# Performance work log

Measured on AMD Instinct MI355X. Metric: run time of the kernel, lower is better.

## Reference

```python
import jax, jax.numpy as jnp
import numpy as np

DT = 0.001          # time step (s)
DX = 5.0            # grid spacing x (m)
DY = 5.0            # grid spacing y (m)
FD_PAD = 2          # accuracy=4 -> stencil half-width 2
PML_W = 20          # default pml_width
PAD = FD_PAD + PML_W
PML_FREQ = 25.0     # default dominant frequency for PML
NZ, NY = 250, 350
N_SHOTS, N_SRC, NT = 4, 1, 48
N_RECV = 100


def _shift(w, k, axis):
    """result[i] = w[i+k] along axis, zero fill outside."""
    pad = [(0, 0)] * w.ndim
    sl = [slice(None)] * w.ndim
    if k >= 0:
        pad[axis] = (0, k)
        sl[axis] = slice(k, None)
    else:
        pad[axis] = (-k, 0)
        sl[axis] = slice(None, k)
    return jnp.pad(w[tuple(sl)], pad)


def _d1(w, axis, d):
    # 4th-order central first derivative
    return (8.0 * (_shift(w, 1, axis) - _shift(w, -1, axis))
            - (_shift(w, 2, axis) - _shift(w, -2, axis))) / (12.0 * d)


def _d2(w, axis, d):
    # 4th-order central second derivative
    return (-(_shift(w, 2, axis) + _shift(w, -2, axis))
            + 16.0 * (_shift(w, 1, axis) + _shift(w, -1, axis))
            - 30.0 * w) / (12.0 * d * d)


def _pml_profiles(n, width, d, dt, vmax, freq):
    """C-PML decay (b) and update (a) coefficients along one axis."""
    x = jnp.arange(n, dtype=jnp.float32)
    frac_lo = jnp.clip((FD_PAD + width - x) / width, 0.0, 1.0)
    frac_hi = jnp.clip((x - (n - 1 - FD_PAD - width)) / width, 0.0, 1.0)
    frac = jnp.maximum(frac_lo, frac_hi)          # 0 interior -> 1 at edge
    sigma = 3.0 * vmax * jnp.log(1000.0) / (2.0 * width * d) * frac * frac
    alpha = jnp.pi * freq * (1.0 - frac)
    b = jnp.exp(-(sigma + alpha) * dt)
    a = sigma / (sigma + alpha + 1e-9) * (b - 1.0)
    return a.astype(jnp.float32), b.astype(jnp.float32)


def setup_inputs() -> dict:
    key = jax.random.key(0)
    k1, k2, k3, k4, k5, k6, k7 = jax.random.split(key, 7)
    v = 1500.0 + 1000.0 * jax.random.uniform(k1, (NZ, NY), jnp.float32)
    scatter = 0.1 * jax.random.normal(k2, (NZ, NY), jnp.float32)
    source_amplitudes = jax.random.normal(k3, (N_SHOTS, N_SRC, NT), jnp.float32)
    source_locations = jnp.stack([
        jax.random.randint(k4, (N_SHOTS, N_SRC), 0, NZ),
        jax.random.randint(k5, (N_SHOTS, N_SRC), 0, NY)], axis=-1)
    receiver_locations = jnp.stack([
        jax.random.randint(k6, (N_SHOTS, N_RECV), 0, NZ),
        jax.random.randint(k7, (N_SHOTS, N_RECV), 0, NY)], axis=-1)
    return {"v": v, "scatter": scatter, "source_amplitudes": source_amplitudes,
            "source_locations": source_locations,
            "receiver_locations": receiver_locations}


def reference(v, scatter, source_amplitudes, source_locations, receiver_locations):
    vp = jnp.pad(v, PAD, mode='edge')              # replicate-pad velocity
    sp = jnp.pad(scatter, PAD)                     # zero-pad scatter
    nx, ny = vp.shape
    vmax = jax.lax.stop_gradient(jnp.max(jnp.abs(v)))
    ax, bx = _pml_profiles(nx, PML_W, DX, DT, vmax, PML_FREQ)
    ay, by = _pml_profiles(ny, PML_W, DY, DT, vmax, PML_FREQ)
    ax, bx = ax[:, None], bx[:, None]              # broadcast over y
    ay, by = ay[None, :], by[None, :]              # broadcast over x
    v2dt2 = vp * vp * (DT * DT)

    n, n_src, nt = source_amplitudes.shape
    sl = source_locations + PAD
    rl = receiver_locations + PAD
    shot = jnp.arange(n)[:, None]
    sx, sy = sl[..., 0], sl[..., 1]
    rx, ry = rl[..., 0], rl[..., 1]

    z = jnp.zeros((n, nx, ny), v.dtype)
    carry0 = (z,) * 12
    amps = jnp.moveaxis(source_amplitudes, -1, 0)  # [nt, shot, src]

    def pml_laplacian(wfc, px, py, zx, zy):
        px = bx * px + ax * _d1(wfc, 1, DX)
        py = by * py + ay * _d1(wfc, 2, DY)
        tx = _d2(wfc, 1, DX) + _d1(px, 1, DX)
        ty = _d2(wfc, 2, DY) + _d1(py, 2, DY)
        zx = bx * zx + ax * tx
        zy = by * zy + ay * ty
        return tx + zx + ty + zy, px, py, zx, zy

    def step(carry, amp):
        wfc, wfp, px, py, zx, zy, wsc, wpsc, pxs, pys, zxs, zys = carry
        lap, px, py, zx, zy = pml_laplacian(wfc, px, py, zx, zy)
        wfn = v2dt2 * lap + 2.0 * wfc - wfp
        wfn = wfn.at[shot, sx, sy].add(v2dt2[sx, sy] * amp)
        lapsc, pxs, pys, zxs, zys = pml_laplacian(wsc, pxs, pys, zxs, zys)
        wfnsc = (v2dt2 * lapsc + 2.0 * wsc - wpsc
                 + 2.0 * vp * sp * (DT * DT) * lap)   # Born scattering source
        rec = wfnsc[shot, rx, ry]                      # [shot, receiver]
        return (wfn, wfc, px, py, zx, zy,
                wfnsc, wsc, pxs, pys, zxs, zys), rec

    _, recs = jax.lax.scan(step, carry0, amps)
    receiver_amplitudes = jnp.moveaxis(recs, 0, -1)    # [shot, receiver, time]
    return receiver_amplitudes
```

## Files before the change

kernel.cpp:

```cpp
#include <hip/hip_runtime.h>

#define DTF   0.001f
#define NZV   250
#define NYV   350
#define NX    294
#define NYW   394
#define PADC  22
#define NSHOT 4
#define NTS   48
#define NRECV 100
#define NCELL (NX*NYW)
#define NTOT  (NSHOT*NCELL)
#define XBL   22
#define XBH   (NX-22)
#define YBH   (NYW-22)
#define NB    44
#define PXSZ  (NSHOT*NB*NYW)
#define PYSZ  (NSHOT*NX*NB)
#define NSB   ((NTOT+255)/256)
#define GB    2

__device__ __forceinline__ int xbi(int i) {
    return ((unsigned)i < XBL) ? i : ((i >= XBH && i < NX) ? i-(NX-NB) : -1);
}
__device__ __forceinline__ int ybi(int j) {
    return ((unsigned)j < XBL) ? j : ((j >= YBH && j < NYW) ? j-(NYW-NB) : -1);
}

__device__ __forceinline__ float ldz(const float* __restrict__ w, int i, int j) {
    return ((unsigned)i < (unsigned)NX && (unsigned)j < (unsigned)NYW) ? w[i*NYW + j] : 0.f;
}
__device__ __forceinline__ float d1x(const float* __restrict__ w, int i, int j) {
    return (8.f*(ldz(w,i+1,j) - ldz(w,i-1,j)) - (ldz(w,i+2,j) - ldz(w,i-2,j))) * (1.f/60.f);
}
__device__ __forceinline__ float d1y(const float* __restrict__ w, int i, int j) {
    return (8.f*(ldz(w,i,j+1) - ldz(w,i,j-1)) - (ldz(w,i,j+2) - ldz(w,i,j-2))) * (1.f/60.f);
}
__device__ __forceinline__ float d2x(const float* __restrict__ w, int i, int j, float cc) {
    return (-(ldz(w,i+2,j)+ldz(w,i-2,j)) + 16.f*(ldz(w,i+1,j)+ldz(w,i-1,j)) - 30.f*cc) * (1.f/300.f);
}
__device__ __forceinline__ float d2y(const float* __restrict__ w, int i, int j, float cc) {
    return (-(ldz(w,i,j+2)+ldz(w,i,j-2)) + 16.f*(ldz(w,i,j+1)+ldz(w,i,j-1)) - 30.f*cc) * (1.f/300.f);
}

__global__ void k_vmax(const float* __restrict__ v, unsigned* __restrict__ vmx) {
    __shared__ float sm[256];
    float m = 0.f;
    for (int idx = blockIdx.x*256 + threadIdx.x; idx < NZV*NYV; idx += gridDim.x*256)
        m = fmaxf(m, fabsf(v[idx]));
    sm[threadIdx.x] = m; __syncthreads();
    for (int o = 128; o > 0; o >>= 1) {
        if (threadIdx.x < o) sm[threadIdx.x] = fmaxf(sm[threadIdx.x], sm[threadIdx.x+o]);
        __syncthreads();
    }
    if (threadIdx.x == 0) atomicMax(vmx, __float_as_uint(sm[0]));
}

__global__ void k_prep(const float* __restrict__ v, const float* __restrict__ sc,
                       float* __restrict__ v2dt2, float* __restrict__ sterm) {
    int c = blockIdx.x*blockDim.x + threadIdx.x;
    if (c >= NCELL) return;
    int i = c / NYW, j = c - (c / NYW)*NYW;
    int iz = min(max(i - PADC, 0), NZV-1);
    int iy = min(max(j - PADC, 0), NYV-1);
    float vv = v[iz*NYV + iy];
    v2dt2[c] = vv*vv*(DTF*DTF);
    float sp = 0.f;
    if (i >= PADC && i < PADC+NZV && j >= PADC && j < PADC+NYV)
        sp = sc[(i-PADC)*NYV + (j-PADC)];
    sterm[c] = 2.f*vv*sp*(DTF*DTF);
}

__device__ __forceinline__ void prof1(int x, int n, float d, float vmax, float* a, float* b) {
    float fl = fminf(fmaxf((float)(2 + 20 - x)/20.f, 0.f), 1.f);
    float fh = fminf(fmaxf((float)(x - (n - 23))/20.f, 0.f), 1.f);
    float fr = fmaxf(fl, fh);
    float sigma = 3.f*vmax*logf(1000.f)/(2.f*20.f*d)*fr*fr;
    float alpha = 3.14159265358979f*25.f*(1.f - fr);
    float bb = expf(-(sigma+alpha)*DTF);
    *a = sigma/(sigma+alpha+1e-9f)*(bb-1.f);
    *b = bb;
}

__global__ void k_prof(const unsigned* __restrict__ vmx,
                       float* __restrict__ axv, float* __restrict__ bxv,
                       float* __restrict__ ayv, float* __restrict__ byv) {
    int x = threadIdx.x;
    float vmax = __uint_as_float(vmx[0]);
    if (x < NX)  prof1(x, NX,  5.0f, vmax, &axv[x], &bxv[x]);
    if (x < NYW) prof1(x, NYW, 5.0f, vmax, &ayv[x], &byv[x]);
}

__global__ __launch_bounds__(256) void k_fstep(
    const float* __restrict__ wf,   float* __restrict__ wold,
    const float* __restrict__ wsf,  float* __restrict__ wsold,
    const float* __restrict__ pxo,  float* __restrict__ pxn,
    const float* __restrict__ pyo,  float* __restrict__ pyn,
    const float* __restrict__ pxso, float* __restrict__ pxsn,
    const float* __restrict__ pyso, float* __restrict__ pysn,
    float* __restrict__ zx,  float* __restrict__ zy,
    float* __restrict__ zxs, float* __restrict__ zys,
    const float* __restrict__ v2, const float* __restrict__ st,
    const float* __restrict__ axv, const float* __restrict__ bxv,
    const float* __restrict__ ayv, const float* __restrict__ byv,
    const float* __restrict__ amp, const int* __restrict__ sloc,
    const int* __restrict__ rloc, float* __restrict__ out, int t)
{
    int bid = blockIdx.x;
    if (bid >= NSB) {
        if (t == 0) return;
        int g = (bid - NSB)*256 + threadIdx.x;
        if (g >= NSHOT*NRECV) return;
        int s = g / NRECV, rr = g - s*NRECV;
        int ri = rloc[(s*NRECV+rr)*2+0] + PADC;
        int rj = rloc[(s*NRECV+rr)*2+1] + PADC;
        out[(s*NRECV+rr)*NTS + (t-1)] = wsf[s*NCELL + ri*NYW + rj];
        return;
    }
    int c = bid*256 + threadIdx.x;
    if (c >= NTOT) return;
    int s = c / NCELL; int r = c - s*NCELL;
    int i = r / NYW;   int j = r - i*NYW;

    const float* w  = wf  + s*NCELL;
    const float* ww = wsf + s*NCELL;

    float wc  = w[r];
    float wsc = ww[r];

    float tx  = d2x(w,  i, j, wc);
    float txs = d2x(ww, i, j, wsc);
    float ty  = d2y(w,  i, j, wc);
    float tys = d2y(ww, i, j, wsc);

    int ib = xbi(i);
    int jb = ybi(j);

    if (i <= XBL+1 || i >= XBH-2) {
        float pv[5], pvs[5];
        #pragma unroll
        for (int k = 0; k < 5; ++k) {
            int ik = i + k - 2; int b = xbi(ik);
            float p = 0.f, ps = 0.f;
            if (b >= 0) {
                float bxk = bxv[ik], axk = axv[ik];
                int o = (s*NB + b)*NYW + j;
                p  = bxk*pxo[o]  + axk*d1x(w,  ik, j);
                ps = bxk*pxso[o] + axk*d1x(ww, ik, j);
            }
            pv[k] = p; pvs[k] = ps;
        }
        tx  += (8.f*(pv[3]-pv[1])  - (pv[4]-pv[0]))  * (1.f/60.f);
        txs += (8.f*(pvs[3]-pvs[1]) - (pvs[4]-pvs[0])) * (1.f/60.f);
        if (ib >= 0) {
            int o = (s*NB + ib)*NYW + j;
            pxn[o] = pv[2]; pxsn[o] = pvs[2];
        }
    }

    if (j <= XBL+1 || j >= YBH-2) {
        float pv[5], pvs[5];
        #pragma unroll
        for (int k = 0; k < 5; ++k) {
            int jk = j + k - 2; int b = ybi(jk);
            float p = 0.f, ps = 0.f;
            if (b >= 0) {
                float byk = byv[jk], ayk = ayv[jk];
                int o = (s*NX + i)*NB + b;
                p  = byk*pyo[o]  + ayk*d1y(w,  i, jk);
                ps = byk*pyso[o] + ayk*d1y(ww, i, jk);
            }
            pv[k] = p; pvs[k] = ps;
        }
        ty  += (8.f*(pv[3]-pv[1])  - (pv[4]-pv[0]))  * (1.f/60.f);
        tys += (8.f*(pvs[3]-pvs[1]) - (pvs[4]-pvs[0])) * (1.f/60.f);
        if (jb >= 0) {
            int o = (s*NX + i)*NB + jb;
            pyn[o] = pv[2]; pysn[o] = pvs[2];
        }
    }

    float zxv = 0.f, zyv = 0.f, zxsv = 0.f, zysv = 0.f;
    if (ib >= 0) {
        int o = (s*NB + ib)*NYW + j;
        float bx = bxv[i], ax = axv[i];
        zxv  = bx*zx[o]  + ax*tx;  zx[o]  = zxv;
        zxsv = bx*zxs[o] + ax*txs; zxs[o] = zxsv;
    }
    if (jb >= 0) {
        int o = (s*NX + i)*NB + jb;
        float by = byv[j], ay = ayv[j];
        zyv  = by*zy[o]  + ay*ty;  zy[o]  = zyv;
        zysv = by*zys[o] + ay*tys; zys[o] = zysv;
    }

    float lap  = tx + zxv + ty + zyv;
    float laps = txs + zxsv + tys + zysv;
    float vd   = v2[r];
    float wn   = vd*lap + 2.f*wc - wold[c];
    if (i == sloc[s*2] + PADC && j == sloc[s*2+1] + PADC)
        wn += vd * amp[s*NTS + t];
    float wsn = vd*laps + 2.f*wsc - wsold[c] + st[r]*lap;
    wold[c]  = wn;
    wsold[c] = wsn;
}

__global__ void k_gtail(const float* __restrict__ wsn, const int* __restrict__ rloc,
                        float* __restrict__ out) {
    int g = blockIdx.x*blockDim.x + threadIdx.x;
    if (g >= NSHOT*NRECV) return;
    int s = g / NRECV, rr = g - s*NRECV;
    int ri = rloc[(s*NRECV+rr)*2+0] + PADC;
    int rj = rloc[(s*NRECV+rr)*2+1] + PADC;
    out[(s*NRECV+rr)*NTS + (NTS-1)] = wsn[s*NCELL + ri*NYW + rj];
}

extern "C" void kernel_launch(void* const* d_in, const int* in_sizes, int n_in,
                              void* d_out, int out_size, void* d_ws, size_t ws_size,
                              hipStream_t stream) {
    const float* v    = (const float*)d_in[0];
    const float* scat = (const float*)d_in[1];
    const float* amp  = (const float*)d_in[2];
    const int*   sloc = (const int*)d_in[3];
    const int*   rloc = (const int*)d_in[4];
    float* out = (float*)d_out;
    float* ws  = (float*)d_ws;

    const size_t F = (size_t)NTOT;
    float* wA   = ws;
    float* wB   = wA + F;
    float* sA   = wB + F;
    float* sB   = sA + F;
    float* pxA  = sB + F;
    float* pxB  = pxA + PXSZ;
    float* pxsA = pxB + PXSZ;
    float* pxsB = pxsA + PXSZ;
    float* zx   = pxsB + PXSZ;
    float* zxs  = zx + PXSZ;
    float* pyA  = zxs + PXSZ;
    float* pyB  = pyA + PYSZ;
    float* pysA = pyB + PYSZ;
    float* pysB = pysA + PYSZ;
    float* zy   = pysB + PYSZ;
    float* zys  = zy + PYSZ;
    float* vmxf = zys + PYSZ;
    float* v2   = vmxf + 1;
    float* st   = v2 + NCELL;
    float* axv  = st + NCELL;
    float* bxv  = axv + NX;
    float* ayv  = bxv + NX;
    float* byv  = ayv + NYW;
    unsigned* vmx = (unsigned*)vmxf;

    size_t zero_floats = 4*F + 6*(size_t)PXSZ + 6*(size_t)PYSZ + 1;
    hipMemsetAsync(ws, 0, zero_floats*sizeof(float), stream);

    hipLaunchKernelGGL(k_vmax, dim3(64), dim3(256), 0, stream, v, vmx);
    hipLaunchKernelGGL(k_prep, dim3((NCELL+255)/256), dim3(256), 0, stream, v, scat, v2, st);
    hipLaunchKernelGGL(k_prof, dim3(1), dim3(512), 0, stream, vmx, axv, bxv, ayv, byv);

    float* wc  = wA;  float* wp  = wB;
    float* scc = sA;  float* scp = sB;
    float* pxc = pxA; float* pxn = pxB;
    float* pyc = pyA; float* pyn = pyB;
    float* pxsc = pxsA; float* pxsn = pxsB;
    float* pysc = pysA; float* pysn = pysB;

    for (int t = 0; t < NTS; ++t) {
        hipLaunchKernelGGL(k_fstep, dim3(NSB + GB), dim3(256), 0, stream,
                           wc, wp, scc, scp,
                           pxc, pxn, pyc, pyn, pxsc, pxsn, pysc, pysn,
                           zx, zy, zxs, zys,
                           v2, st, axv, bxv, ayv, byv,
                           amp, sloc, rloc, out, t);
        float* tmp;
        tmp = wc;  wc  = wp;  wp  = tmp;
        tmp = scc; scc = scp; scp = tmp;
        tmp = pxc; pxc = pxn; pxn = tmp;
        tmp = pyc; pyc = pyn; pyn = tmp;
        tmp = pxsc; pxsc = pxsn; pxsn = tmp;
        tmp = pysc; pysc = pysn; pysn = tmp;
    }
    hipLaunchKernelGGL(k_gtail, dim3(2), dim3(256), 0, stream, scc, rloc, out);
}
```

Baseline: 602.8 us.

## Compute four adjacent y-cells per thread to reuse stencil loads in registers

Each thread of the step kernel now handles four consecutive y-cells of one row. It loads a shared row window into registers and reuses it for the y second derivative and the y PML derivatives, instead of issuing separate bounds-checked loads per cell. This cuts the number of threads and the redundant neighbour loads, but raises register pressure, leaves threads uncoalesced across the strided j groups, and adds a wide workspace offset for the vmax slot.

```diff
diff --git a/kernel.cpp b/kernel.cpp
--- a/kernel.cpp
+++ b/kernel.cpp
@@ -17,8 +17,12 @@
 #define NB    44
 #define PXSZ  (NSHOT*NB*NYW)
 #define PYSZ  (NSHOT*NX*NB)
-#define NSB   ((NTOT+255)/256)
+#define NTHR  256
+#define NJG   99
+#define WITEMS (NSHOT*NX*NJG)
+#define NSB2  ((WITEMS+255)/256)
 #define GB    2
+#define BARF  1024
 
 __device__ __forceinline__ int xbi(int i) {
     return ((unsigned)i < XBL) ? i : ((i >= XBH && i < NX) ? i-(NX-NB) : -1);
@@ -26,21 +30,18 @@
 __device__ __forceinline__ int ybi(int j) {
     return ((unsigned)j < XBL) ? j : ((j >= YBH && j < NYW) ? j-(NYW-NB) : -1);
 }
-
 __device__ __forceinline__ float ldz(const float* __restrict__ w, int i, int j) {
     return ((unsigned)i < (unsigned)NX && (unsigned)j < (unsigned)NYW) ? w[i*NYW + j] : 0.f;
 }
-__device__ __forceinline__ float d1x(const float* __restrict__ w, int i, int j) {
-    return (8.f*(ldz(w,i+1,j) - ldz(w,i-1,j)) - (ldz(w,i+2,j) - ldz(w,i-2,j))) * (1.f/60.f);
-}
-__device__ __forceinline__ float d1y(const float* __restrict__ w, int i, int j) {
-    return (8.f*(ldz(w,i,j+1) - ldz(w,i,j-1)) - (ldz(w,i,j+2) - ldz(w,i,j-2))) * (1.f/60.f);
-}
-__device__ __forceinline__ float d2x(const float* __restrict__ w, int i, int j, float cc) {
-    return (-(ldz(w,i+2,j)+ldz(w,i-2,j)) + 16.f*(ldz(w,i+1,j)+ldz(w,i-1,j)) - 30.f*cc) * (1.f/300.f);
-}
-__device__ __forceinline__ float d2y(const float* __restrict__ w, int i, int j, float cc) {
-    return (-(ldz(w,i,j+2)+ldz(w,i,j-2)) + 16.f*(ldz(w,i,j+1)+ldz(w,i,j-1)) - 30.f*cc) * (1.f/300.f);
+__device__ __forceinline__ void prof1(int x, int n, float d, float vmax, float* a, float* b) {
+    float fl = fminf(fmaxf((float)(2 + 20 - x)/20.f, 0.f), 1.f);
+    float fh = fminf(fmaxf((float)(x - (n - 23))/20.f, 0.f), 1.f);
+    float fr = fmaxf(fl, fh);
+    float sigma = 3.f*vmax*logf(1000.f)/(2.f*20.f*d)*fr*fr;
+    float alpha = 3.14159265358979f*25.f*(1.f - fr);
+    float bb = expf(-(sigma+alpha)*DTF);
+    *a = sigma/(sigma+alpha+1e-9f)*(bb-1.f);
+    *b = bb;
 }
 
 __global__ void k_vmax(const float* __restrict__ v, unsigned* __restrict__ vmx) {
@@ -71,17 +72,6 @@
     sterm[c] = 2.f*vv*sp*(DTF*DTF);
 }
 
-__device__ __forceinline__ void prof1(int x, int n, float d, float vmax, float* a, float* b) {
-    float fl = fminf(fmaxf((float)(2 + 20 - x)/20.f, 0.f), 1.f);
-    float fh = fminf(fmaxf((float)(x - (n - 23))/20.f, 0.f), 1.f);
-    float fr = fmaxf(fl, fh);
-    float sigma = 3.f*vmax*logf(1000.f)/(2.f*20.f*d)*fr*fr;
-    float alpha = 3.14159265358979f*25.f*(1.f - fr);
-    float bb = expf(-(sigma+alpha)*DTF);
-    *a = sigma/(sigma+alpha+1e-9f)*(bb-1.f);
-    *b = bb;
-}
-
 __global__ void k_prof(const unsigned* __restrict__ vmx,
                        float* __restrict__ axv, float* __restrict__ bxv,
                        float* __restrict__ ayv, float* __restrict__ byv) {
@@ -91,7 +81,7 @@
     if (x < NYW) prof1(x, NYW, 5.0f, vmax, &ayv[x], &byv[x]);
 }
 
-__global__ __launch_bounds__(256) void k_fstep(
+__global__ __launch_bounds__(256) void k_fstep4(
     const float* __restrict__ wf,   float* __restrict__ wold,
     const float* __restrict__ wsf,  float* __restrict__ wsold,
     const float* __restrict__ pxo,  float* __restrict__ pxn,
@@ -107,9 +97,9 @@
     const int* __restrict__ rloc, float* __restrict__ out, int t)
 {
     int bid = blockIdx.x;
-    if (bid >= NSB) {
+    if (bid >= NSB2) {
         if (t == 0) return;
-        int g = (bid - NSB)*256 + threadIdx.x;
+        int g = (bid - NSB2)*256 + threadIdx.x;
         if (g >= NSHOT*NRECV) return;
         int s = g / NRECV, rr = g - s*NRECV;
         int ri = rloc[(s*NRECV+rr)*2+0] + PADC;
@@ -117,92 +107,141 @@
         out[(s*NRECV+rr)*NTS + (t-1)] = wsf[s*NCELL + ri*NYW + rj];
         return;
     }
-    int c = bid*256 + threadIdx.x;
-    if (c >= NTOT) return;
-    int s = c / NCELL; int r = c - s*NCELL;
-    int i = r / NYW;   int j = r - i*NYW;
+    int g = bid*256 + threadIdx.x;
+    if (g >= WITEMS) return;
+    int s  = g / (NX*NJG);
+    int rm = g - s*(NX*NJG);
+    int i  = rm / NJG;
+    int jg = rm - i*NJG;
+    int j0 = jg*4;
 
     const float* w  = wf  + s*NCELL;
     const float* ww = wsf + s*NCELL;
 
-    float wc  = w[r];
-    float wsc = ww[r];
-
-    float tx  = d2x(w,  i, j, wc);
-    float txs = d2x(ww, i, j, wsc);
-    float ty  = d2y(w,  i, j, wc);
-    float tys = d2y(ww, i, j, wsc);
-
-    int ib = xbi(i);
-    int jb = ybi(j);
-
+    const bool ybt = (jg <= 5 || jg >= 92);
+
+    float cw[12], cs[12];
+    if (ybt) {
+        #pragma unroll
+        for (int m = 0; m < 12; ++m) { cw[m] = ldz(w, i, j0-4+m); cs[m] = ldz(ww, i, j0-4+m); }
+    } else {
+        cw[0]=cw[1]=cw[10]=cw[11]=0.f; cs[0]=cs[1]=cs[10]=cs[11]=0.f;
+        #pragma unroll
+        for (int m = 0; m < 8; ++m) { cw[2+m] = ldz(w, i, j0-2+m); cs[2+m] = ldz(ww, i, j0-2+m); }
+    }
+    float am2[4], am1[4], ap1[4], ap2[4], bm2[4], bm1[4], bp1[4], bp2[4];
+    #pragma unroll
+    for (int k = 0; k < 4; ++k) {
+        int j = j0 + k;
+        am2[k]=ldz(w,i-2,j); am1[k]=ldz(w,i-1,j); ap1[k]=ldz(w,i+1,j); ap2[k]=ldz(w,i+2,j);
+        bm2[k]=ldz(ww,i-2,j); bm1[k]=ldz(ww,i-1,j); bp1[k]=ldz(ww,i+1,j); bp2[k]=ldz(ww,i+2,j);
+    }
+
+    float tx[4], ty[4], txs[4], tys[4];
+    #pragma unroll
+    for (int k = 0; k < 4; ++k) {
+        tx[k]  = (-(ap2[k]+am2[k]) + 16.f*(ap1[k]+am1[k]) - 30.f*cw[k+4]) * (1.f/300.f);
+        txs[k] = (-(bp2[k]+bm2[k]) + 16.f*(bp1[k]+bm1[k]) - 30.f*cs[k+4]) * (1.f/300.f);
+        ty[k]  = (-(cw[k+6]+cw[k+2]) + 16.f*(cw[k+5]+cw[k+3]) - 30.f*cw[k+4]) * (1.f/300.f);
+        tys[k] = (-(cs[k+6]+cs[k+2]) + 16.f*(cs[k+5]+cs[k+3]) - 30.f*cs[k+4]) * (1.f/300.f);
+    }
+
+    const int ib = xbi(i);
     if (i <= XBL+1 || i >= XBH-2) {
-        float pv[5], pvs[5];
         #pragma unroll
-        for (int k = 0; k < 5; ++k) {
-            int ik = i + k - 2; int b = xbi(ik);
-            float p = 0.f, ps = 0.f;
-            if (b >= 0) {
-                float bxk = bxv[ik], axk = axv[ik];
-                int o = (s*NB + b)*NYW + j;
-                p  = bxk*pxo[o]  + axk*d1x(w,  ik, j);
-                ps = bxk*pxso[o] + axk*d1x(ww, ik, j);
+        for (int k = 0; k < 4; ++k) {
+            int j = j0 + k;
+            if (j >= NYW) continue;
+            float wx[9], wsx[9];
+            #pragma unroll
+            for (int m = 0; m < 9; ++m) { wx[m] = ldz(w, i-4+m, j); wsx[m] = ldz(ww, i-4+m, j); }
+            float pv[5], pvs[5];
+            #pragma unroll
+            for (int kk = 0; kk < 5; ++kk) {
+                int ik = i + kk - 2; int b = xbi(ik);
+                float p = 0.f, ps = 0.f;
+                if (b >= 0) {
+                    float bxk = bxv[ik], axk = axv[ik];
+                    int o = (s*NB + b)*NYW + j;
+                    float d1  = (8.f*(wx[kk+3]-wx[kk+1])  - (wx[kk+4]-wx[kk]))  * (1.f/60.f);
+                    float d1s = (8.f*(wsx[kk+3]-wsx[kk+1]) - (wsx[kk+4]-wsx[kk])) * (1.f/60.f);
+                    p  = bxk*pxo[o]  + axk*d1;
+                    ps = bxk*pxso[o] + axk*d1s;
+                }
+                pv[kk] = p; pvs[kk] = ps;
             }
-            pv[k] = p; pvs[k] = ps;
+            tx[k]  += (8.f*(pv[3]-pv[1])  - (pv[4]-pv[0]))  * (1.f/60.f);
+            txs[k] += (8.f*(pvs[3]-pvs[1]) - (pvs[4]-pvs[0])) * (1.f/60.f);
+            if (ib >= 0) {
+                int o = (s*NB + ib)*NYW + j;
+                pxn[o] = pv[2]; pxsn[o] = pvs[2];
+            }
         }
-        tx  += (8.f*(pv[3]-pv[1])  - (pv[4]-pv[0]))  * (1.f/60.f);
-        txs += (8.f*(pvs[3]-pvs[1]) - (pvs[4]-pvs[0])) * (1.f/60.f);
+    }
+
+    if (ybt) {
+        #pragma unroll
+        for (int k = 0; k < 4; ++k) {
+            int j = j0 + k;
+            if (j >= NYW) continue;
+            if (j <= XBL+1 || j >= YBH-2) {
+                float pv[5], pvs[5];
+                #pragma unroll
+                for (int m = 0; m < 5; ++m) {
+                    int jk = j + m - 2; int b = ybi(jk);
+                    float p = 0.f, ps = 0.f;
+                    if (b >= 0) {
+                        float byk = byv[jk], ayk = ayv[jk];
+                        int o = (s*NX + i)*NB + b;
+                        float d1  = (8.f*(cw[k+m+3]-cw[k+m+1]) - (cw[k+m+4]-cw[k+m])) * (1.f/60.f);
+                        float d1s = (8.f*(cs[k+m+3]-cs[k+m+1]) - (cs[k+m+4]-cs[k+m])) * (1.f/60.f);
+                        p  = byk*pyo[o]  + ayk*d1;
+                        ps = byk*pyso[o] + ayk*d1s;
+                    }
+                    pv[m] = p; pvs[m] = ps;
+                }
+                ty[k]  += (8.f*(pv[3]-pv[1])  - (pv[4]-pv[0]))  * (1.f/60.f);
+                tys[k] += (8.f*(pvs[3]-pvs[1]) - (pvs[4]-pvs[0])) * (1.f/60.f);
+                int jb = ybi(j);
+                if (jb >= 0) {
+                    int o = (s*NX + i)*NB + jb;
+                    pyn[o] = pv[2]; pysn[o] = pvs[2];
+                }
+            }
+        }
+    }
+
+    const int si = sloc[s*2] + PADC, sj = sloc[s*2+1] + PADC;
+    #pragma unroll
+    for (int k = 0; k < 4; ++k) {
+        int j = j0 + k;
+        if (j >= NYW) continue;
+        int r = i*NYW + j;
+        int c = s*NCELL + r;
+        float zxv = 0.f, zxsv = 0.f;
         if (ib >= 0) {
             int o = (s*NB + ib)*NYW + j;
-            pxn[o] = pv[2]; pxsn[o] = pvs[2];
+            float bx = bxv[i], ax = axv[i];
+            zxv  = bx*zx[o]  + ax*tx[k];  zx[o]  = zxv;
+            zxsv = bx*zxs[o] + ax*txs[k]; zxs[o] = zxsv;
         }
-    }
-
-    if (j <= XBL+1 || j >= YBH-2) {
-        float pv[5], pvs[5];
-        #pragma unroll
-        for (int k = 0; k < 5; ++k) {
-            int jk = j + k - 2; int b = ybi(jk);
-            float p = 0.f, ps = 0.f;
-            if (b >= 0) {
-                float byk = byv[jk], ayk = ayv[jk];
-                int o = (s*NX + i)*NB + b;
-                p  = byk*pyo[o]  + ayk*d1y(w,  i, jk);
-                ps = byk*pyso[o] + ayk*d1y(ww, i, jk);
-            }
-            pv[k] = p; pvs[k] = ps;
-        }
-        ty  += (8.f*(pv[3]-pv[1])  - (pv[4]-pv[0]))  * (1.f/60.f);
-        tys += (8.f*(pvs[3]-pvs[1]) - (pvs[4]-pvs[0])) * (1.f/60.f);
+        float zyv = 0.f, zysv = 0.f;
+        int jb = ybi(j);
         if (jb >= 0) {
             int o = (s*NX + i)*NB + jb;
-            pyn[o] = pv[2]; pysn[o] = pvs[2];
+            float by = byv[j], ay = ayv[j];
+            zyv  = by*zy[o]  + ay*ty[k];  zy[o]  = zyv;
+            zysv = by*zys[o] + ay*tys[k]; zys[o] = zysv;
         }
-    }
-
-    float zxv = 0.f, zyv = 0.f, zxsv = 0.f, zysv = 0.f;
-    if (ib >= 0) {
-        int o = (s*NB + ib)*NYW + j;
-        float bx = bxv[i], ax = axv[i];
-        zxv  = bx*zx[o]  + ax*tx;  zx[o]  = zxv;
-        zxsv = bx*zxs[o] + ax*txs; zxs[o] = zxsv;
-    }
-    if (jb >= 0) {
-        int o = (s*NX + i)*NB + jb;
-        float by = byv[j], ay = ayv[j];
-        zyv  = by*zy[o]  + ay*ty;  zy[o]  = zyv;
-        zysv = by*zys[o] + ay*tys; zys[o] = zysv;
-    }
-
-    float lap  = tx + zxv + ty + zyv;
-    float laps = txs + zxsv + tys + zysv;
-    float vd   = v2[r];
-    float wn   = vd*lap + 2.f*wc - wold[c];
-    if (i == sloc[s*2] + PADC && j == sloc[s*2+1] + PADC)
-        wn += vd * amp[s*NTS + t];
-    float wsn = vd*laps + 2.f*wsc - wsold[c] + st[r]*lap;
-    wold[c]  = wn;
-    wsold[c] = wsn;
+        float lap  = tx[k] + zxv + ty[k] + zyv;
+        float laps = txs[k] + zxsv + tys[k] + zysv;
+        float vd   = v2[r];
+        float wn   = vd*lap + 2.f*cw[k+4] - wold[c];
+        if (i == si && j == sj) wn += vd * amp[s*NTS + t];
+        float wsn = vd*laps + 2.f*cs[k+4] - wsold[c] + st[r]*lap;
+        wold[c]  = wn;
+        wsold[c] = wsn;
+    }
 }
 
 __global__ void k_gtail(const float* __restrict__ wsn, const int* __restrict__ rloc,
@@ -226,8 +265,9 @@
     float* out = (float*)d_out;
     float* ws  = (float*)d_ws;
 
+    float* base = ws + BARF;
     const size_t F = (size_t)NTOT;
-    float* wA   = ws;
+    float* wA   = base;
     float* wB   = wA + F;
     float* sA   = wB + F;
     float* sB   = sA + F;
@@ -243,16 +283,15 @@
     float* pysB = pysA + PYSZ;
     float* zy   = pysB + PYSZ;
     float* zys  = zy + PYSZ;
-    float* vmxf = zys + PYSZ;
-    float* v2   = vmxf + 1;
+    float* v2   = zys + PYSZ;
     float* st   = v2 + NCELL;
     float* axv  = st + NCELL;
     float* bxv  = axv + NX;
     float* ayv  = bxv + NX;
     float* byv  = ayv + NYW;
-    unsigned* vmx = (unsigned*)vmxf;
-
-    size_t zero_floats = 4*F + 6*(size_t)PXSZ + 6*(size_t)PYSZ + 1;
+    unsigned* vmx = (unsigned*)ws;
+
+    size_t zero_floats = BARF + 4*F + 6*(size_t)PXSZ + 6*(size_t)PYSZ;
     hipMemsetAsync(ws, 0, zero_floats*sizeof(float), stream);
 
     hipLaunchKernelGGL(k_vmax, dim3(64), dim3(256), 0, stream, v, vmx);
@@ -267,7 +306,7 @@
     float* pysc = pysA; float* pysn = pysB;
 
     for (int t = 0; t < NTS; ++t) {
-        hipLaunchKernelGGL(k_fstep, dim3(NSB + GB), dim3(256), 0, stream,
+        hipLaunchKernelGGL(k_fstep4, dim3(NSB2 + GB), dim3(256), 0, stream,
                            wc, wp, scc, scp,
                            pxc, pxn, pyc, pyn, pxsc, pxsn, pysc, pysn,
                            zx, zy, zxs, zys,
```

Measured after the change: 1.298 ms. +115.3%, slower.
